# Optimization experiments

Measured on AMD Instinct MI355X. Metric: run time of the kernel, lower is better.

Reference implementation:

```python
import jax, jax.numpy as jnp
import numpy as np

SPARSITY = 0.8
LOCAL_WINDOW = 64


def setup_inputs() -> dict:
    key = jax.random.key(0)
    k1, k2 = jax.random.split(key)
    B, H, S = 2, 8, 2048
    attention_scores = jax.random.normal(k1, (B, H, S, S), dtype=jnp.float32)
    rand_u = jax.random.uniform(k2, (B, H, S, S), dtype=jnp.float32)
    return {"attention_scores": attention_scores, "rand_u": rand_u}


def reference(attention_scores, rand_u):
    B, H, S, _ = attention_scores.shape
    dt = attention_scores.dtype
    half = LOCAL_WINDOW // 2
    k = max(1, int(S * (1.0 - SPARSITY)))

    idx = jnp.arange(S)
    # local window mask: row i covers columns [max(0,i-half), min(S,i+half))
    local = ((idx[None, :] >= idx[:, None] - half) & (idx[None, :] < idx[:, None] + half)).astype(dt)  # (S,S)

    # global mask: topk over head-averaged importance, shared across heads
    importance = attention_scores.mean(axis=1)  # (B,S,S)
    _, top_g = jax.lax.top_k(importance, k)  # (B,S,k)
    gmask = jnp.zeros((B, S, S), dtype=dt).at[
        jnp.arange(B)[:, None, None], jnp.arange(S)[None, :, None], top_g
    ].set(1.0)

    # random sparsification mask
    random_mask = (rand_u < (1.0 - SPARSITY)).astype(dt)

    combined = ((local[None, None, :, :] + gmask[:, None, :, :] + random_mask) > 0).astype(dt)

    # sparsity enforcement: per-row topk of masked scores -> binary mask
    masked = attention_scores * combined
    _, top_f = jax.lax.top_k(masked, k)  # (B,H,S,k)
    final = jnp.zeros((B, H, S, S), dtype=dt).at[
        jnp.arange(B)[:, None, None, None],
        jnp.arange(H)[None, :, None, None],
        jnp.arange(S)[None, None, :, None],
        top_f,
    ].set(1.0)
    return final
```

## Files before the change

### kernel.cpp

```cpp
#include <hip/hip_runtime.h>
#include <cstdint>
#include <cstddef>

#define S_LEN   2048
#define N_HEADS 8
#define N_BATCH 2
#define TOPK    409
#define HALF_WIN 32
#define NT      256
#define PT      8
#define KEY_P0  0x80000000u
#define KEY_N0  0x7FFFFFFFu

__device__ __forceinline__ unsigned mono(float f) {
  unsigned u = __float_as_uint(f);
  return (u & 0x80000000u) ? ~u : (u | 0x80000000u);
}

__device__ __forceinline__ unsigned mbcnt64(unsigned long long m) {
  return __builtin_amdgcn_mbcnt_hi((unsigned)(m >> 32),
         __builtin_amdgcn_mbcnt_lo((unsigned)m, 0u));
}


struct SelScratch {
  unsigned hist[256];
  unsigned sbuf[256];
  unsigned bk[2];
};

__device__ __forceinline__ unsigned block_sum(unsigned c, SelScratch* s) {
  const int t = threadIdx.x;
  s->sbuf[t] = c;
  __syncthreads();
  #pragma unroll
  for (int d = 128; d > 0; d >>= 1) {
    if (t < d) s->sbuf[t] += s->sbuf[t + d];
    __syncthreads();
  }
  unsigned r = s->sbuf[0];
  __syncthreads();
  return r;
}

__device__ void radix_select(const unsigned* keys, int k, unsigned n0, unsigned n1,
                             SelScratch* s, unsigned* T_out, int* kk_out) {
  const int t = threadIdx.x;
  unsigned prefix = 0, done = 0;
  unsigned kk = (unsigned)k;
  #pragma unroll
  for (int shift = 24; shift >= 0; shift -= 8) {
    s->hist[t] = 0;
    __syncthreads();
    if (t == 0 && n0 != 0 && (KEY_P0 & done) == prefix)
      atomicAdd(&s->hist[(KEY_P0 >> shift) & 255u], n0);
    if (t == 1 && n1 != 0 && (KEY_N0 & done) == prefix)
      atomicAdd(&s->hist[(KEY_N0 >> shift) & 255u], n1);
    #pragma unroll
    for (int q = 0; q < PT; ++q) {
      unsigned kj = keys[t + NT * q];
      if (kj != KEY_P0 && kj != KEY_N0 && (kj & done) == prefix)
        atomicAdd(&s->hist[(kj >> shift) & 255u], 1u);
    }
    __syncthreads();
    s->sbuf[t] = s->hist[t];
    __syncthreads();
    for (int d = 1; d < 256; d <<= 1) {
      unsigned a = (t + d < 256) ? s->sbuf[t + d] : 0u;
      __syncthreads();
      s->sbuf[t] += a;
      __syncthreads();
    }
    unsigned suf_ge = s->sbuf[t];
    unsigned suf_gt = (t < 255) ? s->sbuf[t + 1] : 0u;
    if (suf_gt < kk && kk <= suf_ge) {
      s->bk[0] = (unsigned)t;
      s->bk[1] = kk - suf_gt;
    }
    __syncthreads();
    prefix |= s->bk[0] << shift;
    kk = s->bk[1];
    done |= 0xFFu << shift;
    __syncthreads();
  }
  *T_out = prefix;
  *kk_out = (int)kk;
}

__device__ __forceinline__ int stable_rank_base(int c, SelScratch* s) {
  const int t = threadIdx.x;
  s->sbuf[t] = (unsigned)c;
  __syncthreads();
  for (int d = 1; d < 256; d <<= 1) {
    unsigned a = (t >= d) ? s->sbuf[t - d] : 0u;
    __syncthreads();
    s->sbuf[t] += a;
    __syncthreads();
  }
  int base = (t == 0) ? 0 : (int)s->sbuf[t - 1];
  __syncthreads();
  return base;
}

__global__ __launch_bounds__(NT) void k_gmask(const float* __restrict__ scores,
                                              unsigned* __restrict__ gwords) {
  __shared__ __align__(16) unsigned keys[S_LEN];
  __shared__ SelScratch scr;
  __shared__ __align__(4) unsigned char gb[NT];
  const int t = threadIdx.x;
  const int blk = blockIdx.x;
  const int b = blk >> 11;
  const int i = blk & 2047;
  const size_t base = (((size_t)b * N_HEADS) * S_LEN + i) * S_LEN;

  unsigned c0 = 0, c1 = 0;
  #pragma unroll
  for (int s4 = 0; s4 < 2; ++s4) {
    const int j0 = (t + NT * s4) * 4;
    float4 a = *(const float4*)(scores + base + j0);
    #pragma unroll
    for (int h = 1; h < N_HEADS; ++h) {
      float4 x = *(const float4*)(scores + base + (size_t)h * S_LEN * S_LEN + j0);
      a.x += x.x; a.y += x.y; a.z += x.z; a.w += x.w;
    }
    unsigned kqa[4] __attribute__((aligned(16)));
    kqa[0] = mono(a.x); kqa[1] = mono(a.y); kqa[2] = mono(a.z); kqa[3] = mono(a.w);
    #pragma unroll
    for (int q = 0; q < 4; ++q) {
      c0 += (kqa[q] == KEY_P0);
      c1 += (kqa[q] == KEY_N0);
    }
    *(uint4*)(&keys[j0]) = *(uint4*)kqa;
  }
  __syncthreads();

  unsigned ns = block_sum(c0 | (c1 << 16), &scr);
  unsigned T; int kk;
  radix_select(keys, TOPK, ns & 0xFFFFu, ns >> 16, &scr, &T, &kk);

  int c = 0;
  #pragma unroll
  for (int e = 0; e < PT; ++e) c += (keys[t * PT + e] == T);
  int r = stable_rank_base(c, &scr);

  unsigned byte = 0;
  #pragma unroll
  for (int e = 0; e < PT; ++e) {
    unsigned kj = keys[t * PT + e];
    bool sel;
    if (kj > T)       sel = true;
    else if (kj == T) { sel = (r < kk); ++r; }
    else              sel = false;
    byte |= (unsigned)sel << e;
  }
  gb[t] = (unsigned char)byte;
  __syncthreads();
  if (t < 64) gwords[(size_t)blk * 64 + t] = ((const unsigned*)gb)[t];
}


__device__ __forceinline__ void radix_range(const unsigned (&keys)[32], unsigned kk0,
                                            bool pos, unsigned* h, int l,
                                            unsigned& T_ret, unsigned& kk_ret) {
  unsigned prefix = 0, done = 0, kk = kk0;
  unsigned T = 0;
  bool resolved = false;
  #pragma unroll
  for (int pass = 0; pass < 4; ++pass) {
    const int shift = 24 - 8 * pass;
    *(uint4*)&h[l * 4] = make_uint4(0, 0, 0, 0);
    __threadfence_block();
    #pragma unroll
    for (int q = 0; q < 32; ++q) {
      unsigned kj = keys[q];
      bool in = pos ? (kj > KEY_P0) : (kj < KEY_N0);
      if (in && (kj & done) == prefix)
        atomicAdd(&h[(kj >> shift) & 255u], 1u);
    }
    __threadfence_block();
    uint4 hv = *(const uint4*)&h[l * 4];
    unsigned s3 = hv.w;
    unsigned s2 = hv.z + s3;
    unsigned s1 = hv.y + s2;
    unsigned s0 = hv.x + s1;
    unsigned inc = s0;
    #pragma unroll
    for (int d = 1; d < 64; d <<= 1) {
      unsigned o = __shfl_down(inc, d);
      inc += (l + d < 64) ? o : 0u;
    }
    const unsigned tail = inc - s0;
    const unsigned ge[4] = {s0 + tail, s1 + tail, s2 + tail, s3 + tail};
    const unsigned gt[4] = {s1 + tail, s2 + tail, s3 + tail, tail};
    unsigned packed = 0;
    bool found = false;
    #pragma unroll
    for (int q = 0; q < 4; ++q) {
      if (gt[q] < kk && kk <= ge[q]) {
        packed = ((unsigned)(4 * l + q) << 24) | ((ge[q] - gt[q]) << 12) | (kk - gt[q]);
        found = true;
      }
    }
    unsigned long long bal = __ballot(found);
    int srcl = __ffsll((long long)bal) - 1;
    packed = __shfl(packed, srcl);
    const unsigned cnt = (packed >> 12) & 0xFFFu;
    kk = packed & 0xFFFu;
    prefix |= (packed >> 24) << shift;
    done |= 0xFFu << shift;
    if (cnt == 1u) {
      unsigned cand = 0;
      #pragma unroll
      for (int q = 0; q < 32; ++q) {
        unsigned kj = keys[q];
        bool in = pos ? (kj > KEY_P0) : (kj < KEY_N0);
        if (in && (kj & done) == prefix) cand = kj;
      }
      #pragma unroll
      for (int d = 1; d < 64; d <<= 1) cand |= __shfl_xor(cand, d);
      T = cand;
      resolved = true;
      break;
    }
  }
  if (!resolved) T = prefix;
  T_ret = T;
  kk_ret = kk;
}

__global__ __launch_bounds__(256) void k_final(const float* __restrict__ scores,
                                               const float* __restrict__ randu,
                                               const unsigned* __restrict__ gwords,
                                               float* __restrict__ out) {
  __shared__ __align__(16) unsigned hist[4][256];
  __shared__ unsigned gm[4][64];
  const int l = threadIdx.x & 63;
  const int w = threadIdx.x >> 6;
  const int row = blockIdx.x * 4 + w;
  const int i = row & 2047;
  const int b = row >> 14;
  const size_t base = (size_t)row * S_LEN;
  const float thr = (float)(1.0 - 0.8);
  unsigned* h = hist[w];
  unsigned* g = gm[w];

  g[l] = gwords[((size_t)(b << 11) + i) * 64 + l];

  unsigned keys[32];
  unsigned c0 = 0, c1 = 0, cp = 0;
  #pragma unroll
  for (int s = 0; s < 8; ++s) {
    const int j0 = 256 * s + 4 * l;
    float4 sc = *(const float4*)(scores + base + j0);
    float4 ru = *(const float4*)(randu + base + j0);
    const unsigned gmw = g[8 * s + (l >> 3)];
    const float scv[4] = {sc.x, sc.y, sc.z, sc.w};
    const float ruv[4] = {ru.x, ru.y, ru.z, ru.w};
    #pragma unroll
    for (int e = 0; e < 4; ++e) {
      const int j = j0 + e;
      bool loc = (j >= i - HALF_WIN) && (j < i + HALF_WIN);
      bool gbit = (gmw >> (4 * (l & 7) + e)) & 1u;
      bool rnd = ruv[e] < thr;
      unsigned u = __float_as_uint(scv[e]);
      unsigned key;
      if (loc || gbit || rnd) key = (u & 0x80000000u) ? ~u : (u | 0x80000000u);
      else                    key = (u >> 31) ? KEY_N0 : KEY_P0;
      c0 += (key == KEY_P0);
      c1 += (key == KEY_N0);
      cp += (key > KEY_P0);
      keys[4 * s + e] = key;
    }
  }

  unsigned cs = c0 | (c1 << 16);
  #pragma unroll
  for (int d = 1; d < 64; d <<= 1) {
    cs += __shfl_xor(cs, d);
    cp += __shfl_xor(cp, d);
  }
  const unsigned n0 = cs & 0xFFFFu, n1 = cs >> 16, np = cp;

  unsigned T, kk;
  if (TOPK <= np) {
    radix_range(keys, TOPK, true, h, l, T, kk);
  } else if (TOPK <= np + n0) {
    T = KEY_P0; kk = TOPK - np;
  } else if (TOPK <= np + n0 + n1) {
    T = KEY_N0; kk = TOPK - np - n0;
  } else {
    radix_range(keys, TOPK - np - n0 - n1, false, h, l, T, kk);
  }

  unsigned S_before = 0;
  #pragma unroll
  for (int s = 0; s < 8; ++s) {
    unsigned long long bal[4];
    unsigned mb[4], own[4];
    #pragma unroll
    for (int e = 0; e < 4; ++e) {
      bal[e] = __ballot(keys[4 * s + e] == T);
      mb[e]  = mbcnt64(bal[e]);
      own[e] = (unsigned)((bal[e] >> l) & 1ull);
    }
    const unsigned cross = S_before + mb[0] + mb[1] + mb[2] + mb[3];
    float v[4] __attribute__((aligned(16)));
    unsigned run = 0;
    #pragma unroll
    for (int e = 0; e < 4; ++e) {
      unsigned kj = keys[4 * s + e];
      bool sel = (kj > T) || (kj == T && (cross + run) < kk);
      run += own[e];
      v[e] = sel ? 1.0f : 0.0f;
    }
    *(float4*)(out + base + 256 * s + 4 * l) = *(const float4*)v;
    S_before += (unsigned)(__popcll(bal[0]) + __popcll(bal[1]) +
                           __popcll(bal[2]) + __popcll(bal[3]));
  }
}

extern "C" void kernel_launch(void* const* d_in, const int* in_sizes, int n_in,
                              void* d_out, int out_size, void* d_ws, size_t ws_size,
                              hipStream_t stream) {
  const float* scores = (const float*)d_in[0];
  const float* randu  = (const float*)d_in[1];
  float* out = (float*)d_out;
  unsigned* gwords = (unsigned*)d_ws;
  k_gmask<<<N_BATCH * S_LEN, NT, 0, stream>>>(scores, gwords);
  k_final<<<N_BATCH * N_HEADS * S_LEN / 4, 256, 0, stream>>>(scores, randu, gwords, out);
}
```

Measured before the change: 232.9 us.

## Fold local window into gmask words and simplify key building and tie selection

The local-window mask is OR-ed into the per-row global mask bitwords when k_gmask writes them, so k_final no longer evaluates the window test per element. Key construction becomes a branchless XOR form, and the per-row counts now come from wave ballots and popcounts instead of a shuffle reduction. The final selection takes a fast path when a whole 256-column chunk lies fully inside or outside the tie budget, skipping mbcnt prefix work. The cost is more ballots in the key loop, and correctness depends on the window bits matching the reference across heads and rows.

Measured after the change: 224.5 us. 1.04x faster.

```diff
diff --git a/kernel.cpp b/kernel.cpp
--- a/kernel.cpp
+++ b/kernel.cpp
@@ -155,7 +155,19 @@
   }
   gb[t] = (unsigned char)byte;
   __syncthreads();
-  if (t < 64) gwords[(size_t)blk * 64 + t] = ((const unsigned*)gb)[t];
+  if (t < 64) {
+    unsigned wv = ((const unsigned*)gb)[t];
+    int s0 = i - HALF_WIN - 32 * t;
+    int e0 = i + HALF_WIN - 32 * t;
+    s0 = s0 < 0 ? 0 : (s0 > 32 ? 32 : s0);
+    e0 = e0 < 0 ? 0 : (e0 > 32 ? 32 : e0);
+    unsigned lm = 0;
+    if (e0 > s0) {
+      unsigned hiM = (e0 == 32) ? 0xFFFFFFFFu : ((1u << e0) - 1u);
+      lm = hiM & ~((1u << s0) - 1u);
+    }
+    gwords[(size_t)blk * 64 + t] = wv | lm;
+  }
 }
 
 
@@ -246,8 +258,9 @@
 
   g[l] = gwords[((size_t)(b << 11) + i) * 64 + l];
 
+  const int bitbase = 4 * (l & 7);
   unsigned keys[32];
-  unsigned c0 = 0, c1 = 0, cp = 0;
+  unsigned np = 0, n0 = 0, n1 = 0;
   #pragma unroll
   for (int s = 0; s < 8; ++s) {
     const int j0 = 256 * s + 4 * l;
@@ -258,28 +271,16 @@
     const float ruv[4] = {ru.x, ru.y, ru.z, ru.w};
     #pragma unroll
     for (int e = 0; e < 4; ++e) {
-      const int j = j0 + e;
-      bool loc = (j >= i - HALF_WIN) && (j < i + HALF_WIN);
-      bool gbit = (gmw >> (4 * (l & 7) + e)) & 1u;
-      bool rnd = ruv[e] < thr;
-      unsigned u = __float_as_uint(scv[e]);
-      unsigned key;
-      if (loc || gbit || rnd) key = (u & 0x80000000u) ? ~u : (u | 0x80000000u);
-      else                    key = (u >> 31) ? KEY_N0 : KEY_P0;
-      c0 += (key == KEY_P0);
-      c1 += (key == KEY_N0);
-      cp += (key > KEY_P0);
+      const unsigned u = __float_as_uint(scv[e]);
+      const unsigned m = (unsigned)((int)u >> 31) | 0x80000000u;
+      const bool comb = (((gmw >> (bitbase + e)) & 1u) != 0u) | (ruv[e] < thr);
+      const unsigned key = (comb ? u : (u & 0x80000000u)) ^ m;
       keys[4 * s + e] = key;
-    }
-  }
-
-  unsigned cs = c0 | (c1 << 16);
-  #pragma unroll
-  for (int d = 1; d < 64; d <<= 1) {
-    cs += __shfl_xor(cs, d);
-    cp += __shfl_xor(cp, d);
-  }
-  const unsigned n0 = cs & 0xFFFFu, n1 = cs >> 16, np = cp;
+      np += (unsigned)__popcll(__ballot(key > KEY_P0));
+      n0 += (unsigned)__popcll(__ballot(key == KEY_P0));
+      n1 += (unsigned)__popcll(__ballot(key == KEY_N0));
+    }
+  }
 
   unsigned T, kk;
   if (TOPK <= np) {
@@ -292,30 +293,45 @@
     radix_range(keys, TOPK - np - n0 - n1, false, h, l, T, kk);
   }
 
-  unsigned S_before = 0;
+  unsigned S_tot = 0;
   #pragma unroll
   for (int s = 0; s < 8; ++s) {
-    unsigned long long bal[4];
-    unsigned mb[4], own[4];
+    unsigned long long beq[4];
+    unsigned pe[4];
     #pragma unroll
     for (int e = 0; e < 4; ++e) {
-      bal[e] = __ballot(keys[4 * s + e] == T);
-      mb[e]  = mbcnt64(bal[e]);
-      own[e] = (unsigned)((bal[e] >> l) & 1ull);
-    }
-    const unsigned cross = S_before + mb[0] + mb[1] + mb[2] + mb[3];
+      beq[e] = __ballot(keys[4 * s + e] == T);
+      pe[e] = (unsigned)__popcll(beq[e]);
+    }
+    const unsigned th = pe[0] + pe[1] + pe[2] + pe[3];
     float v[4] __attribute__((aligned(16)));
-    unsigned run = 0;
-    #pragma unroll
-    for (int e = 0; e < 4; ++e) {
-      unsigned kj = keys[4 * s + e];
-      bool sel = (kj > T) || (kj == T && (cross + run) < kk);
-      run += own[e];
-      v[e] = sel ? 1.0f : 0.0f;
-    }
+    if (S_tot + th <= kk) {
+      #pragma unroll
+      for (int e = 0; e < 4; ++e)
+        v[e] = (keys[4 * s + e] >= T) ? 1.0f : 0.0f;
+    } else if (S_tot >= kk) {
+      #pragma unroll
+      for (int e = 0; e < 4; ++e)
+        v[e] = (keys[4 * s + e] > T) ? 1.0f : 0.0f;
+    } else {
+      unsigned mb[4], own[4];
+      #pragma unroll
+      for (int e = 0; e < 4; ++e) {
+        mb[e]  = mbcnt64(beq[e]);
+        own[e] = (unsigned)((beq[e] >> l) & 1ull);
+      }
+      const unsigned cross = S_tot + mb[0] + mb[1] + mb[2] + mb[3];
+      unsigned run = 0;
+      #pragma unroll
+      for (int e = 0; e < 4; ++e) {
+        unsigned kj = keys[4 * s + e];
+        bool sel = (kj > T) || (kj == T && (cross + run) < kk);
+        run += own[e];
+        v[e] = sel ? 1.0f : 0.0f;
+      }
+    }
+    S_tot += th;
     *(float4*)(out + base + 256 * s + 4 * l) = *(const float4*)v;
-    S_before += (unsigned)(__popcll(bal[0]) + __popcll(bal[1]) +
-                           __popcll(bal[2]) + __popcll(bal[3]));
   }
 }
 
```
